# Kernel optimization log

Measured on AMD Instinct MI355X. Metric: run time of the kernel, lower is better.

The kernel has to match this reference:

```python
import jax, jax.numpy as jnp
import numpy as np

BATCH, SEQ, EMBED = 8, 1024, 2048
HEADS, LATENT = 16, 512
HEAD_DIM = EMBED // HEADS            # 128
NOPE = HEAD_DIM // 4                 # 32 (qk_rope_dim=96 is even, no adjust)
ROPE_D = HEAD_DIM - NOPE             # 96
THETA = 10000.0


def _rope_tables(seq_len):
    # matches torch: freqs over arange(0, rope_dim, 2)/rope_dim
    freqs = 1.0 / THETA ** (jnp.arange(0, ROPE_D, 2, dtype=jnp.float32) / ROPE_D)
    emb = jnp.arange(seq_len, dtype=jnp.float32)[:, None] * freqs[None, :]  # [S, ROPE_D//2]
    return jnp.cos(emb), jnp.sin(emb)


def _apply_rope(x, cos, sin):
    # x: [B,H,S,D]; cos/sin: [S,D//2]. NOTE: original concatenates halves (non-interleaved output).
    xe, xo = x[..., ::2], x[..., 1::2]
    return jnp.concatenate([xe * cos - xo * sin, xo * cos + xe * sin], axis=-1)


def setup_inputs() -> dict:
    key = jax.random.key(0)
    ks = jax.random.split(key, 5)
    x = jax.random.normal(ks[0], (BATCH, SEQ, EMBED), jnp.float32)
    Wq = jax.random.normal(ks[1], (EMBED, EMBED), jnp.float32) * 0.02
    Wkv_down = jax.random.normal(ks[2], (EMBED, LATENT), jnp.float32) * 0.02
    Wk_up = jax.random.normal(ks[3], (LATENT, EMBED), jnp.float32) * 0.02
    Wv_up = jax.random.normal(ks[4], (LATENT, EMBED), jnp.float32) * 0.02
    return {"x": x, "Wq": Wq, "Wkv_down": Wkv_down, "Wk_up": Wk_up, "Wv_up": Wv_up}


def reference(x, Wq, Wkv_down, Wk_up, Wv_up):
    B, S, E = x.shape
    # projections (weights stored [in, out], equivalent to nn.Linear math)
    q = (x @ Wq).reshape(B, S, HEADS, HEAD_DIM).transpose(0, 2, 1, 3)   # [B,H,S,D]
    q_nope, q_rope = q[..., :NOPE], q[..., NOPE:]
    c_kv = x @ Wkv_down                                                  # [B,S,latent]
    k = (c_kv @ Wk_up).reshape(B, S, HEADS, HEAD_DIM).transpose(0, 2, 1, 3)
    v = (c_kv @ Wv_up).reshape(B, S, HEADS, HEAD_DIM).transpose(0, 2, 1, 3)
    k_nope, k_rope = k[..., :NOPE], k[..., NOPE:]

    cos, sin = _rope_tables(S)
    q_rope = _apply_rope(q_rope, cos, sin)
    k_rope = _apply_rope(k_rope, cos, sin)

    qf = jnp.concatenate([q_nope, q_rope], axis=-1)
    kf = jnp.concatenate([k_nope, k_rope], axis=-1)

    scale = jnp.float32(1.0 / np.sqrt(HEAD_DIM))
    scores = jnp.einsum('bhqd,bhkd->bhqk', qf, kf) * scale
    causal = jnp.triu(jnp.ones((S, S), dtype=bool), k=1)  # past_length=0
    scores = jnp.where(causal, -jnp.inf, scores)
    weights = jax.nn.softmax(scores, axis=-1)
    out = jnp.einsum('bhqk,bhkd->bhqd', weights, v)
    return out.transpose(0, 2, 1, 3).reshape(B, S, E)
```

## Files before the change

### kernel.cpp

```cpp
#include <hip/hip_runtime.h>
#include <stdint.h>

typedef unsigned short u16;
typedef __bf16 bf16x8 __attribute__((ext_vector_type(8)));
typedef float    f32x4 __attribute__((ext_vector_type(4)));
typedef unsigned short u16x8 __attribute__((ext_vector_type(8)));
typedef unsigned short u16x4 __attribute__((ext_vector_type(4)));

#define BB 8
#define SS 1024
#define EE 2048
#define HH 16
#define DD 128

__device__ __forceinline__ u16 f2bf(float f){
  union { float f; unsigned u; } v; v.f = f;
  unsigned r = v.u + 0x7FFFu + ((v.u >> 16) & 1u);
  return (u16)(r >> 16);
}
__device__ __forceinline__ float bf2f(u16 h){
  union { unsigned u; float f; } v; v.u = ((unsigned)h) << 16;
  return v.f;
}
__device__ __forceinline__ bf16x8 ld8(const u16* p){
  return __builtin_bit_cast(bf16x8, *(const u16x8*)p);
}

typedef __attribute__((address_space(1))) const unsigned int gas_u32;
typedef __attribute__((address_space(3))) unsigned int las_u32;
__device__ __forceinline__ void g2l16(const u16* g, u16* l){
  __builtin_amdgcn_global_load_lds((gas_u32*)g, (las_u32*)l, 16, 0, 0);
}

#define BARRIER() asm volatile("s_barrier" ::: "memory")
#define VMC(n)    asm volatile("s_waitcnt vmcnt(" #n ")" ::: "memory")

__global__ __launch_bounds__(256) void cvt_f32_bf16(const float* __restrict__ in,
                                                    u16* __restrict__ out, int n){
  int i = (blockIdx.x*256 + threadIdx.x)*8;
  if (i >= n) return;
  float4 v0 = *(const float4*)(in + i);
  float4 v1 = *(const float4*)(in + i + 4);
  u16x8 o;
  o[0]=f2bf(v0.x); o[1]=f2bf(v0.y); o[2]=f2bf(v0.z); o[3]=f2bf(v0.w);
  o[4]=f2bf(v1.x); o[5]=f2bf(v1.y); o[6]=f2bf(v1.z); o[7]=f2bf(v1.w);
  *(u16x8*)(out + i) = o;
}

__global__ __launch_bounds__(256) void transposeW(const float* __restrict__ W,
                                                  u16* __restrict__ Wt, int K, int N){
  __shared__ float t[32][33];
  int c = threadIdx.x & 31, r = threadIdx.x >> 5;
  int bx = blockIdx.x, by = blockIdx.y;
  #pragma unroll
  for (int i = 0; i < 32; i += 8)
    t[r+i][c] = W[(size_t)(by*32 + r + i)*N + bx*32 + c];
  __syncthreads();
  #pragma unroll
  for (int i = 0; i < 32; i += 8)
    Wt[(size_t)(bx*32 + r + i)*K + by*32 + c] = f2bf(t[c][r+i]);
}

__global__ __launch_bounds__(256) void rope_tables(float* __restrict__ cosb,
                                                   float* __restrict__ sinb){
  int i = blockIdx.x*256 + threadIdx.x;
  if (i >= SS*48) return;
  int s = i / 48, j = i % 48;
  float freq = powf(10000.0f, -((float)(2*j)) / 96.0f);
  float e = (float)s * freq;
  cosb[i] = cosf(e);
  sinb[i] = sinf(e);
}

__global__ __launch_bounds__(256) void rope_apply(u16* __restrict__ buf,
                                                  const float* __restrict__ cosb,
                                                  const float* __restrict__ sinb){
  int t = blockIdx.x*256 + threadIdx.x;
  int row = t >> 4, h = t & 15, s = row & (SS-1);
  u16* p = buf + (size_t)row*EE + h*DD + 32;
  float e[48], o[48];
  #pragma unroll
  for (int c = 0; c < 12; c++){
    u16x8 v = *(const u16x8*)(p + c*8);
    #pragma unroll
    for (int j = 0; j < 4; j++){
      e[c*4 + j] = bf2f(v[2*j]);
      o[c*4 + j] = bf2f(v[2*j+1]);
    }
  }
  u16 ob[96];
  #pragma unroll
  for (int j = 0; j < 48; j++){
    float cs = cosb[s*48 + j], sn = sinb[s*48 + j];
    ob[j]      = f2bf(e[j]*cs - o[j]*sn);
    ob[48 + j] = f2bf(o[j]*cs + e[j]*sn);
  }
  #pragma unroll
  for (int c = 0; c < 12; c++)
    *(u16x8*)(p + c*8) = *(const u16x8*)(ob + c*8);
}

__global__ __launch_bounds__(256) void gemm_bt(const u16* __restrict__ A,
    const u16* __restrict__ Bt, u16* __restrict__ C, int M, int N, int K){
  __shared__ u16 Al[128*32];
  __shared__ u16 Bl[128*32];
  const int tid = threadIdx.x;
  const int lane = tid & 63, w = tid >> 6;
  const int wr = w >> 1, wc = w & 1;
  const int l15 = lane & 15, l4 = lane >> 4;
  const int bm = blockIdx.y*128, bn = blockIdx.x*128;
  const int srow = tid >> 2;
  const int skc  = (tid & 3) * 8;
  const u16* ga = A  + (size_t)(bm + srow)*K + skc;
  const u16* gb = Bt + (size_t)(bn + srow)*K + skc;
  u16* la = Al + w*512;
  u16* lb = Bl + w*512;
  f32x4 acc[4][4] = {};
  for (int k0 = 0; k0 < K; k0 += 32){
    __syncthreads();
    g2l16(ga + k0,          la);
    g2l16(ga + 64*K + k0,   la + 2048);
    g2l16(gb + k0,          lb);
    g2l16(gb + 64*K + k0,   lb + 2048);
    __syncthreads();
    bf16x8 af[4], bfr[4];
    #pragma unroll
    for (int m = 0; m < 4; m++) af[m]  = ld8(Al + (wr*64 + m*16 + l15)*32 + l4*8);
    #pragma unroll
    for (int n = 0; n < 4; n++) bfr[n] = ld8(Bl + (wc*64 + n*16 + l15)*32 + l4*8);
    #pragma unroll
    for (int m = 0; m < 4; m++)
      #pragma unroll
      for (int n = 0; n < 4; n++)
        acc[m][n] = __builtin_amdgcn_mfma_f32_16x16x32_bf16(af[m], bfr[n], acc[m][n], 0, 0, 0);
  }
  #pragma unroll
  for (int m = 0; m < 4; m++)
    #pragma unroll
    for (int n = 0; n < 4; n++)
      #pragma unroll
      for (int r = 0; r < 4; r++){
        int row = bm + wr*64 + m*16 + l4*4 + r;
        int col = bn + wc*64 + n*16 + l15;
        C[(size_t)row*N + col] = f2bf(acc[m][n][r]);
      }
}

#define AFR(buf, mf, ks) ld8(&AL[buf][wr][((mf)*16 + l15)*64 + ((((ks)*4 + l4) ^ r7) << 3)])
#define BFR(buf, nf, ks) ld8(&BL[buf][wc>>1][(((wc&1)*64 + (nf)*16 + l15))*64 + ((((ks)*4 + l4) ^ r7) << 3)])

#define STAGE_A(buf, h, kt) stage2(aRow, (h), (kt), K, &AL[buf][h][0], wj0)
#define STAGE_B(buf, h, kt) stage2(bRow, (h), (kt), K, &BL[buf][h][0], wj0)

__device__ __forceinline__ void stage2(const u16* rowbase, int h, int kt, int K,
                                       u16* lds, int wj0){
  const u16* g = rowbase + (size_t)h*128*K + kt*64;
  g2l16(g,               lds + wj0*512);
  g2l16(g + (size_t)8*K, lds + wj0*512 + 512);
}

#define PHASE(buf, q, LOADB, STAGE, VM) do{                                        \
  bf16x8 a00 = AFR(buf, 2*(q)  , 0);                                              \
  bf16x8 a01 = AFR(buf, 2*(q)  , 1);                                              \
  bf16x8 a10 = AFR(buf, 2*(q)+1, 0);                                              \
  bf16x8 a11 = AFR(buf, 2*(q)+1, 1);                                              \
  if (LOADB){                                                                      \
    _Pragma("unroll")                                                              \
    for (int nf = 0; nf < 4; nf++){ bq[nf][0]=BFR(buf,nf,0); bq[nf][1]=BFR(buf,nf,1); } \
  }                                                                                \
  STAGE;                                                                           \
  if (VM) VMC(4);                                                                  \
  BARRIER();                                                                       \
  __builtin_amdgcn_s_setprio(1);                                                   \
  _Pragma("unroll")                                                                \
  for (int nf = 0; nf < 4; nf++){                                                  \
    acc[2*(q)][nf]   = __builtin_amdgcn_mfma_f32_16x16x32_bf16(a00, bq[nf][0], acc[2*(q)][nf],0,0,0);   \
    acc[2*(q)+1][nf] = __builtin_amdgcn_mfma_f32_16x16x32_bf16(a10, bq[nf][0], acc[2*(q)+1][nf],0,0,0); \
  }                                                                                \
  _Pragma("unroll")                                                                \
  for (int nf = 0; nf < 4; nf++){                                                  \
    acc[2*(q)][nf]   = __builtin_amdgcn_mfma_f32_16x16x32_bf16(a01, bq[nf][1], acc[2*(q)][nf],0,0,0);   \
    acc[2*(q)+1][nf] = __builtin_amdgcn_mfma_f32_16x16x32_bf16(a11, bq[nf][1], acc[2*(q)+1][nf],0,0,0); \
  }                                                                                \
  __builtin_amdgcn_s_setprio(0);                                                   \
  BARRIER();                                                                       \
  __builtin_amdgcn_sched_barrier(0);                                               \
}while(0)

__global__ __launch_bounds__(512, 2) void gemm8(const u16* __restrict__ A,
    const u16* __restrict__ Bt, u16* __restrict__ C0, u16* __restrict__ C1,
    int K, int Nout, int nsplit, int vt){
  __shared__ u16 AL[2][2][128*64];
  __shared__ u16 BL[2][2][128*64];
  const int tid = threadIdx.x, lane = tid & 63, w = tid >> 6;
  const int wr = w >> 2, wc = w & 3;
  const int l15 = lane & 15, l4 = lane >> 4;
  const int r7 = l15 & 7;
  const int bm = blockIdx.y*256, bn = blockIdx.x*256;
  const int wj0 = w*2;
  const int cswz = (lane & 7) ^ (lane >> 3);
  const u16* aRow = A  + (size_t)(bm + wj0*8 + (lane>>3))*K + cswz*8;
  const u16* bRow = Bt + (size_t)(bn + wj0*8 + (lane>>3))*K + cswz*8;

  const int nkt = K >> 6;
  const int niter = nkt >> 1;

  STAGE_A(0, 0, 0); STAGE_A(0, 1, 0);
  STAGE_B(0, 0, 0); STAGE_B(0, 1, 0);
  STAGE_B(1, 0, 1); STAGE_B(1, 1, 1);
  VMC(4);
  BARRIER();

  f32x4 acc[8][4] = {};
  bf16x8 bq[4][2];

  for (int it = 0; it < niter; ++it){
    const int kto = 2*it + 1;
    int kt2 = 2*it + 2; if (kt2 >= nkt) kt2 -= nkt;
    int kt3 = 2*it + 3; if (kt3 >= nkt) kt3 -= nkt;
    PHASE(0, 0, 1, STAGE_A(1, 0, kto), 0);
    PHASE(0, 1, 0, STAGE_A(1, 1, kto), 0);
    PHASE(0, 2, 0, STAGE_B(0, 0, kt2), 0);
    PHASE(0, 3, 0, STAGE_B(0, 1, kt2), 1);
    PHASE(1, 0, 1, STAGE_A(0, 0, kt2), 0);
    PHASE(1, 1, 0, STAGE_A(0, 1, kt2), 0);
    PHASE(1, 2, 0, STAGE_B(1, 0, kt3), 0);
    PHASE(1, 3, 0, STAGE_B(1, 1, kt3), 1);
  }
  asm volatile("s_waitcnt vmcnt(0)" ::: "memory");

  if (vt && bn >= nsplit){
    const int bcol = bn - nsplit;
    #pragma unroll
    for (int mf = 0; mf < 8; mf++)
      #pragma unroll
      for (int nf = 0; nf < 4; nf++){
        int row0 = bm + wr*128 + mf*16 + l4*4;
        int col  = bcol + wc*64 + nf*16 + l15;
        int bh = (row0 >> 10)*16 + (col >> 7);
        int d  = col & 127;
        int s  = row0 & 1023;
        u16x4 pk;
        #pragma unroll
        for (int r = 0; r < 4; r++) pk[r] = f2bf(acc[mf][nf][r]);
        *(u16x4*)(C1 + (((size_t)(bh*128 + d)) << 10) + s) = pk;
      }
  } else {
    u16* Cd = (bn < nsplit) ? C0 : C1;
    const int bcol = (bn < nsplit) ? bn : bn - nsplit;
    #pragma unroll
    for (int mf = 0; mf < 8; mf++)
      #pragma unroll
      for (int nf = 0; nf < 4; nf++)
        #pragma unroll
        for (int r = 0; r < 4; r++){
          int row = bm + wr*128 + mf*16 + l4*4 + r;
          int col = bcol + wc*64 + nf*16 + l15;
          Cd[(size_t)row*Nout + col] = f2bf(acc[mf][nf][r]);
        }
  }
}

__global__ __launch_bounds__(512) void attn(const u16* __restrict__ qp,
                                            const u16* __restrict__ kp,
                                            const u16* __restrict__ vpT,
                                            float* __restrict__ out){
  __shared__ u16 Kl[2][64*128];
  __shared__ u16 Vl[128*64];
  __shared__ u16 Pl[8][16*72];
  const int tid = threadIdx.x, lane = tid & 63, w = tid >> 6;
  const int l15 = lane & 15, l4 = lane >> 4;
  const int qt = 7 - blockIdx.y;
  const int bh = blockIdx.x;
  const int b = bh >> 4, h = bh & 15;
  const int qbase = qt*128;
  const int qmin = qbase + w*16;
  const float c = 0.12751920700948998f;

  const int kR0 = w*8 + (l4 & 3) + ((lane>>4)==0 ? 0 : 0);
  const size_t rowq = (size_t)(b*SS + qmin + l15)*EE + h*DD;
  bf16x8 qf[4];
  #pragma unroll
  for (int kk = 0; kk < 4; kk++) qf[kk] = ld8(qp + rowq + kk*32 + l4*8);
  #pragma unroll
  for (int kk = 0; kk < 4; kk++) asm volatile("" : "+v"(qf[kk]));

  f32x4 ao[8] = {};
  float mi[4], li[4];
  #pragma unroll
  for (int r = 0; r < 4; r++){ mi[r] = -3e38f; li[r] = 0.0f; }

  const int ntiles = 2*qt + 2;

  #pragma unroll
  for (int q = 0; q < 2; q++){
    int r = w*8 + q*4 + (lane>>4);
    int p = lane & 15;
    g2l16(kp + (size_t)(b*SS + r)*EE + h*DD + ((p ^ (r&7))<<3),
          &Kl[0][0] + (w*128 + q*64)*8);
  }
  VMC(0);

  for (int t = 0; t < ntiles; t++){
    const int kv0 = t*64;
    const int buf = t & 1;
    #pragma unroll
    for (int q = 0; q < 2; q++){
      int d = w*16 + q*8 + (lane>>3);
      int cc = lane & 7;
      g2l16(vpT + (size_t)(bh*DD + d)*SS + kv0 + ((cc ^ (d&7))<<3),
            &Vl[0] + (w*128 + q*64)*8);
    }
    if (t + 1 < ntiles){
      #pragma unroll
      for (int q = 0; q < 2; q++){
        int r = w*8 + q*4 + (lane>>4);
        int p = lane & 15;
        g2l16(kp + (size_t)(b*SS + kv0 + 64 + r)*EE + h*DD + ((p ^ (r&7))<<3),
              &Kl[buf^1][0] + (w*128 + q*64)*8);
      }
      VMC(4);
    } else {
      VMC(2);
    }
    BARRIER();

    const bool part = (kv0 <= qmin + 15);
    float pout[4][4];
    if (part){
      float sv[4][4];
      #pragma unroll
      for (int nt = 0; nt < 4; nt++){
        f32x4 sacc = {};
        #pragma unroll
        for (int kk = 0; kk < 4; kk++){
          bf16x8 kf = ld8(&Kl[buf][0] + (nt*16 + l15)*128 + (((kk*4 + l4) ^ (l15&7))<<3));
          sacc = __builtin_amdgcn_mfma_f32_16x16x32_bf16(qf[kk], kf, sacc, 0, 0, 0);
        }
        #pragma unroll
        for (int r = 0; r < 4; r++) sv[nt][r] = sacc[r];
      }
      if (kv0 + 63 > qmin){
        #pragma unroll
        for (int nt = 0; nt < 4; nt++)
          #pragma unroll
          for (int r = 0; r < 4; r++){
            int qg = qmin + l4*4 + r;
            int kg_ = kv0 + nt*16 + l15;
            if (kg_ > qg) sv[nt][r] = -3e38f;
          }
      }
      #pragma unroll
      for (int r = 0; r < 4; r++){
        float mx = fmaxf(fmaxf(sv[0][r], sv[1][r]), fmaxf(sv[2][r], sv[3][r]));
        #pragma unroll
        for (int off = 1; off < 16; off <<= 1) mx = fmaxf(mx, __shfl_xor(mx, off));
        float mnew = fmaxf(mi[r], mx);
        float mnc = mnew * c;
        float alpha = __builtin_amdgcn_exp2f(__builtin_fmaf(mi[r], c, -mnc));
        float rs = 0.0f;
        #pragma unroll
        for (int nt = 0; nt < 4; nt++){
          float pv = __builtin_amdgcn_exp2f(__builtin_fmaf(sv[nt][r], c, -mnc));
          pout[nt][r] = pv; rs += pv;
        }
        #pragma unroll
        for (int off = 1; off < 16; off <<= 1) rs += __shfl_xor(rs, off);
        li[r] = li[r]*alpha + rs;
        mi[r] = mnew;
        #pragma unroll
        for (int n8 = 0; n8 < 8; n8++) ao[n8][r] *= alpha;
      }
      #pragma unroll
      for (int nt = 0; nt < 4; nt++)
        #pragma unroll
        for (int r = 0; r < 4; r++)
          Pl[w][(l4*4 + r)*72 + nt*16 + l15] = f2bf(pout[nt][r]);
    }
    if (t + 1 < ntiles) VMC(2); else VMC(0);
    BARRIER();
    if (part){
      #pragma unroll
      for (int kk = 0; kk < 2; kk++){
        bf16x8 pa = ld8(&Pl[w][l15*72 + kk*32 + l4*8]);
        #pragma unroll
        for (int n8 = 0; n8 < 8; n8++){
          bf16x8 vf = ld8(&Vl[0] + (n8*16 + l15)*64 + (((kk*4 + l4) ^ (l15&7))<<3));
          ao[n8] = __builtin_amdgcn_mfma_f32_16x16x32_bf16(pa, vf, ao[n8], 0, 0, 0);
        }
      }
    }
    BARRIER();
  }

  #pragma unroll
  for (int r = 0; r < 4; r++){
    float inv = 1.0f / li[r];
    size_t orow = (size_t)(b*SS + qmin + l4*4 + r)*EE + h*DD;
    #pragma unroll
    for (int n8 = 0; n8 < 8; n8++)
      out[orow + n8*16 + l15] = ao[n8][r]*inv;
  }
}

extern "C" void kernel_launch(void* const* d_in, const int* in_sizes, int n_in,
                              void* d_out, int out_size, void* d_ws, size_t ws_size,
                              hipStream_t stream){
  const float* x    = (const float*)d_in[0];
  const float* Wq   = (const float*)d_in[1];
  const float* Wkvd = (const float*)d_in[2];
  const float* Wku  = (const float*)d_in[3];
  const float* Wvu  = (const float*)d_in[4];
  float* out = (float*)d_out;
  char* ws = (char*)d_ws;

  u16*   xb    = (u16*)  (ws);
  u16*   WqT   = (u16*)  (ws +  33554432);
  u16*   WkvdT = (u16*)  (ws +  41943040);
  u16*   WkuT  = (u16*)  (ws +  44040192);
  u16*   WvuT  = (u16*)  (ws +  46137344);
  float* cosb  = (float*)(ws +  48234496);
  float* sinb  = (float*)(ws +  48431104);
  u16*   qp    = (u16*)  (ws +  48627712);
  u16*   ckv   = (u16*)  (ws +  82182144);
  u16*   kp    = (u16*)  (ws +  90570752);
  u16*   vpT   = (u16*)  (ws + 124125184);

  cvt_f32_bf16<<<(BB*SS*EE)/(256*8), 256, 0, stream>>>(x, xb, BB*SS*EE);
  transposeW<<<dim3(EE/32,  EE/32), 256, 0, stream>>>(Wq,   WqT,   EE,  EE);
  transposeW<<<dim3(512/32, EE/32), 256, 0, stream>>>(Wkvd, WkvdT, EE,  512);
  transposeW<<<dim3(EE/32, 512/32), 256, 0, stream>>>(Wku,  WkuT,  512, EE);
  transposeW<<<dim3(EE/32, 512/32), 256, 0, stream>>>(Wvu,  WvuT,  512, EE);
  rope_tables<<<(SS*48 + 255)/256, 256, 0, stream>>>(cosb, sinb);

  gemm8<<<dim3(EE/256, (BB*SS)/256), 512, 0, stream>>>(xb, WqT, qp, qp, EE, EE, EE, 0);
  gemm_bt<<<dim3(512/128, (BB*SS)/128), 256, 0, stream>>>(xb, WkvdT, ckv, BB*SS, 512, EE);
  gemm8<<<dim3(4096/256, (BB*SS)/256), 512, 0, stream>>>(ckv, WkuT, kp, vpT, 512, EE, EE, 1);

  rope_apply<<<(BB*SS*HH)/256, 256, 0, stream>>>(qp, cosb, sinb);
  rope_apply<<<(BB*SS*HH)/256, 256, 0, stream>>>(kp, cosb, sinb);

  attn<<<dim3(BB*HH, SS/128), 512, 0, stream>>>(qp, kp, vpT, out);
}
```

Measured before the change: 325.7 us.

## Double-buffer V in attention, lazy softmax rescale, swizzle P, merge rope launches

The attention kernel now double-buffers the V tile alongside K and prefetches the next K/V tile together, which removes the mid-iteration barrier and vmcnt wait between the softmax and PV phases. Online-softmax rescaling of the accumulator is skipped unless the running max grows past a threshold, so most tiles avoid multiplying the output accumulators. The P scratch buffer drops its padding in favour of an XOR swizzle, and s_setprio is raised around the MFMA sections. The two rope_apply launches are merged into one 2D-grid launch. Costs are more shared memory per block, which may lower occupancy, and a redundant reload on the final tile.

Result: slower. 341.3 us (+4.8%).

```diff
diff --git a/kernel.cpp b/kernel.cpp
--- a/kernel.cpp
+++ b/kernel.cpp
@@ -72,12 +72,14 @@
   sinb[i] = sinf(e);
 }
 
-__global__ __launch_bounds__(256) void rope_apply(u16* __restrict__ buf,
-                                                  const float* __restrict__ cosb,
-                                                  const float* __restrict__ sinb){
+__global__ __launch_bounds__(256) void rope_apply2(u16* __restrict__ qp,
+                                                   u16* __restrict__ kp,
+                                                   const float* __restrict__ cosb,
+                                                   const float* __restrict__ sinb){
+  u16* base = blockIdx.y ? kp : qp;
   int t = blockIdx.x*256 + threadIdx.x;
   int row = t >> 4, h = t & 15, s = row & (SS-1);
-  u16* p = buf + (size_t)row*EE + h*DD + 32;
+  u16* p = base + (size_t)row*EE + h*DD + 32;
   float e[48], o[48];
   #pragma unroll
   for (int c = 0; c < 12; c++){
@@ -266,8 +268,8 @@
                                             const u16* __restrict__ vpT,
                                             float* __restrict__ out){
   __shared__ u16 Kl[2][64*128];
-  __shared__ u16 Vl[128*64];
-  __shared__ u16 Pl[8][16*72];
+  __shared__ u16 Vl[2][128*64];
+  __shared__ u16 Pl[8][16*64];
   const int tid = threadIdx.x, lane = tid & 63, w = tid >> 6;
   const int l15 = lane & 15, l4 = lane >> 4;
   const int qt = 7 - blockIdx.y;
@@ -276,8 +278,8 @@
   const int qbase = qt*128;
   const int qmin = qbase + w*16;
   const float c = 0.12751920700948998f;
-
-  const int kR0 = w*8 + (l4 & 3) + ((lane>>4)==0 ? 0 : 0);
+  const float THR = 62.7f;
+
   const size_t rowq = (size_t)(b*SS + qmin + l15)*EE + h*DD;
   bf16x8 qf[4];
   #pragma unroll
@@ -292,43 +294,42 @@
 
   const int ntiles = 2*qt + 2;
 
+  const int krow = w*8 + (lane>>4);
+  const int kcol = ((lane & 15) ^ (krow & 7)) << 3;
+  const int vd   = w*16 + (lane>>3);
+  const int vcc  = lane & 7;
+
   #pragma unroll
   for (int q = 0; q < 2; q++){
     int r = w*8 + q*4 + (lane>>4);
-    int p = lane & 15;
-    g2l16(kp + (size_t)(b*SS + r)*EE + h*DD + ((p ^ (r&7))<<3),
-          &Kl[0][0] + (w*128 + q*64)*8);
-  }
-  VMC(0);
+    g2l16(kp + (size_t)(b*SS + r)*EE + h*DD + (((lane&15) ^ (r&7))<<3),
+          &Kl[0][0] + w*1024 + q*512);
+    int d = w*16 + q*8 + (lane>>3);
+    g2l16(vpT + (size_t)(bh*DD + d)*SS + ((vcc ^ (d&7))<<3),
+          &Vl[0][0] + w*1024 + q*512);
+  }
 
   for (int t = 0; t < ntiles; t++){
     const int kv0 = t*64;
     const int buf = t & 1;
-    #pragma unroll
-    for (int q = 0; q < 2; q++){
-      int d = w*16 + q*8 + (lane>>3);
-      int cc = lane & 7;
-      g2l16(vpT + (size_t)(bh*DD + d)*SS + kv0 + ((cc ^ (d&7))<<3),
-            &Vl[0] + (w*128 + q*64)*8);
-    }
-    if (t + 1 < ntiles){
+    {
+      const int kvn = (t + 1 < ntiles) ? kv0 + 64 : kv0;
       #pragma unroll
       for (int q = 0; q < 2; q++){
         int r = w*8 + q*4 + (lane>>4);
-        int p = lane & 15;
-        g2l16(kp + (size_t)(b*SS + kv0 + 64 + r)*EE + h*DD + ((p ^ (r&7))<<3),
-              &Kl[buf^1][0] + (w*128 + q*64)*8);
-      }
-      VMC(4);
-    } else {
-      VMC(2);
+        g2l16(kp + (size_t)(b*SS + kvn + r)*EE + h*DD + (((lane&15) ^ (r&7))<<3),
+              &Kl[buf^1][0] + w*1024 + q*512);
+        int d = w*16 + q*8 + (lane>>3);
+        g2l16(vpT + (size_t)(bh*DD + d)*SS + kvn + ((vcc ^ (d&7))<<3),
+              &Vl[buf^1][0] + w*1024 + q*512);
+      }
     }
+    VMC(4);
     BARRIER();
 
-    const bool part = (kv0 <= qmin + 15);
-    float pout[4][4];
-    if (part){
+    if (kv0 <= qmin + 15){
       float sv[4][4];
+      __builtin_amdgcn_s_setprio(1);
       #pragma unroll
       for (int nt = 0; nt < 4; nt++){
         f32x4 sacc = {};
@@ -340,6 +341,7 @@
         #pragma unroll
         for (int r = 0; r < 4; r++) sv[nt][r] = sacc[r];
       }
+      __builtin_amdgcn_s_setprio(0);
       if (kv0 + 63 > qmin){
         #pragma unroll
         for (int nt = 0; nt < 4; nt++)
@@ -350,14 +352,31 @@
             if (kg_ > qg) sv[nt][r] = -3e38f;
           }
       }
+      float mx[4];
+      int need = 0;
       #pragma unroll
       for (int r = 0; r < 4; r++){
-        float mx = fmaxf(fmaxf(sv[0][r], sv[1][r]), fmaxf(sv[2][r], sv[3][r]));
-        #pragma unroll
-        for (int off = 1; off < 16; off <<= 1) mx = fmaxf(mx, __shfl_xor(mx, off));
-        float mnew = fmaxf(mi[r], mx);
-        float mnc = mnew * c;
-        float alpha = __builtin_amdgcn_exp2f(__builtin_fmaf(mi[r], c, -mnc));
+        float m0 = fmaxf(fmaxf(sv[0][r], sv[1][r]), fmaxf(sv[2][r], sv[3][r]));
+        #pragma unroll
+        for (int off = 1; off < 16; off <<= 1) m0 = fmaxf(m0, __shfl_xor(m0, off));
+        mx[r] = m0;
+        need |= (m0 > mi[r] + THR);
+      }
+      if (__any(need)){
+        #pragma unroll
+        for (int r = 0; r < 4; r++){
+          float mnew = fmaxf(mi[r], mx[r]);
+          float alpha = __builtin_amdgcn_exp2f((mi[r] - mnew)*c);
+          mi[r] = mnew;
+          li[r] *= alpha;
+          #pragma unroll
+          for (int n8 = 0; n8 < 8; n8++) ao[n8][r] *= alpha;
+        }
+      }
+      float pout[4][4];
+      #pragma unroll
+      for (int r = 0; r < 4; r++){
+        float mnc = mi[r]*c;
         float rs = 0.0f;
         #pragma unroll
         for (int nt = 0; nt < 4; nt++){
@@ -366,32 +385,30 @@
         }
         #pragma unroll
         for (int off = 1; off < 16; off <<= 1) rs += __shfl_xor(rs, off);
-        li[r] = li[r]*alpha + rs;
-        mi[r] = mnew;
-        #pragma unroll
-        for (int n8 = 0; n8 < 8; n8++) ao[n8][r] *= alpha;
+        li[r] += rs;
       }
       #pragma unroll
       for (int nt = 0; nt < 4; nt++)
         #pragma unroll
-        for (int r = 0; r < 4; r++)
-          Pl[w][(l4*4 + r)*72 + nt*16 + l15] = f2bf(pout[nt][r]);
-    }
-    if (t + 1 < ntiles) VMC(2); else VMC(0);
-    BARRIER();
-    if (part){
+        for (int r = 0; r < 4; r++){
+          int row = l4*4 + r;
+          Pl[w][row*64 + (((nt*2 + (l15>>3)) ^ (row&7))<<3) + (l15&7)] = f2bf(pout[nt][r]);
+        }
+      __builtin_amdgcn_s_setprio(1);
       #pragma unroll
       for (int kk = 0; kk < 2; kk++){
-        bf16x8 pa = ld8(&Pl[w][l15*72 + kk*32 + l4*8]);
+        bf16x8 pa = ld8(&Pl[w][l15*64 + (((kk*4 + l4) ^ (l15&7))<<3)]);
         #pragma unroll
         for (int n8 = 0; n8 < 8; n8++){
-          bf16x8 vf = ld8(&Vl[0] + (n8*16 + l15)*64 + (((kk*4 + l4) ^ (l15&7))<<3));
+          bf16x8 vf = ld8(&Vl[buf][0] + (n8*16 + l15)*64 + (((kk*4 + l4) ^ (l15&7))<<3));
           ao[n8] = __builtin_amdgcn_mfma_f32_16x16x32_bf16(pa, vf, ao[n8], 0, 0, 0);
         }
       }
+      __builtin_amdgcn_s_setprio(0);
     }
     BARRIER();
   }
+  asm volatile("s_waitcnt vmcnt(0)" ::: "memory");
 
   #pragma unroll
   for (int r = 0; r < 4; r++){
@@ -437,8 +454,7 @@
   gemm_bt<<<dim3(512/128, (BB*SS)/128), 256, 0, stream>>>(xb, WkvdT, ckv, BB*SS, 512, EE);
   gemm8<<<dim3(4096/256, (BB*SS)/256), 512, 0, stream>>>(ckv, WkuT, kp, vpT, 512, EE, EE, 1);
 
-  rope_apply<<<(BB*SS*HH)/256, 256, 0, stream>>>(qp, cosb, sinb);
-  rope_apply<<<(BB*SS*HH)/256, 256, 0, stream>>>(kp, cosb, sinb);
+  rope_apply2<<<dim3((BB*SS*HH)/256, 2), 256, 0, stream>>>(qp, kp, cosb, sinb);
 
   attn<<<dim3(BB*HH, SS/128), 512, 0, stream>>>(qp, kp, vpT, out);
 }
```
